# Performance work log

Measured on AMD Instinct MI355X. Metric: run time of the kernel, lower is better.

The kernel has to match this reference:

```python
import jax, jax.numpy as jnp
import numpy as np
from jax import lax

KERNEL_SIZE = 15  # conv padding = kernel_size, kernel width = 2*kernel_size+1


def setup_inputs() -> dict:
    key = jax.random.key(0)
    ks = jax.random.split(key, 11)
    B, T, H, U, KN = 32, 2048, 1024, 1024, 32
    inp = {
        "query": jax.random.normal(ks[0], (1, B, H), dtype=jnp.float32),
        "values": jax.random.normal(ks[1], (B, T, H), dtype=jnp.float32),
        "prev_att": jax.random.uniform(ks[2], (B, 1, T), dtype=jnp.float32),
        "W1_w": jax.random.normal(ks[3], (U, H), dtype=jnp.float32) * 0.02,
        "W1_b": jax.random.normal(ks[4], (U,), dtype=jnp.float32) * 0.02,
        "W2_w": jax.random.normal(ks[5], (U, H), dtype=jnp.float32) * 0.02,
        "W2_b": jax.random.normal(ks[6], (U,), dtype=jnp.float32) * 0.02,
        "V_w": jax.random.normal(ks[7], (1, U), dtype=jnp.float32) * 0.02,
        "V_b": jax.random.normal(ks[8], (1,), dtype=jnp.float32) * 0.02,
        "conv_w": jax.random.normal(ks[9], (KN, 1, 2 * KERNEL_SIZE + 1), dtype=jnp.float32) * 0.02,
        "loc_proj_w": jax.random.normal(ks[10], (U, KN), dtype=jnp.float32) * 0.02,
    }
    return inp


def reference(query, values, prev_att, W1_w, W1_b, W2_w, W2_b, V_w, V_b, conv_w, loc_proj_w):
    # query: [1,B,H] -> [B,H]
    q = jnp.squeeze(query, axis=0)
    hidden_with_time_axis = q[:, None, :]  # [B,1,H]

    # location features: Conv1d over prev attention [B,1,T] -> [B,KN,T]
    loc = lax.conv_general_dilated(
        prev_att, conv_w,
        window_strides=(1,),
        padding=[(KERNEL_SIZE, KERNEL_SIZE)],
        dimension_numbers=("NCH", "OIH", "NCH"),
    )
    # project KN -> units: [B,T,U]
    loc_context = jnp.einsum("bkt,uk->btu", loc, loc_proj_w)

    # W1(values) [B,T,U] + W2(query) [B,1,U] + loc_context [B,T,U]
    sum_1 = (jnp.einsum("bth,uh->btu", values, W1_w) + W1_b
             + jnp.einsum("bh,uh->bu", q, W2_w)[:, None, :] + W2_b
             + loc_context)

    # score: [B,T,1]
    score = jnp.einsum("btu,ou->bto", jnp.tanh(sum_1), V_w) + V_b
    attention_weights = jax.nn.softmax(score, axis=1)  # softmax over time
    context_vector = jnp.sum(attention_weights * values, axis=1)  # [B,H]
    return (context_vector, attention_weights, score)
```

## Files before the change

### kernel.cpp

```cpp
#include <hip/hip_runtime.h>
#include <cstdint>
#include <cstddef>

typedef unsigned short ushort_t;
typedef __attribute__((ext_vector_type(8))) short short8;
typedef __attribute__((ext_vector_type(4))) float floatx4;

#define B_   32
#define T_   2048
#define H_   1024
#define U_   1024
#define KN_  32
#define KEXT 1056
#define BT_  (B_ * T_)

__device__ __forceinline__ unsigned short f2bf(float f) {
    union { float f; unsigned int u; } v; v.f = f;
    unsigned int u = v.u;
    return (unsigned short)((u + 0x7FFFu + ((u >> 16) & 1u)) >> 16);
}
__device__ __forceinline__ float bf2f(unsigned short h) {
    union { unsigned int u; float f; } v; v.u = ((unsigned int)h) << 16;
    return v.f;
}
__device__ __forceinline__ float bflo(unsigned int u) {
    union { unsigned int u; float f; } v; v.u = u << 16; return v.f;
}
__device__ __forceinline__ float bfhi(unsigned int u) {
    union { unsigned int u; float f; } v; v.u = u & 0xffff0000u; return v.f;
}
__device__ __forceinline__ void async_cp16(const void* g, void* l) {
    __builtin_amdgcn_global_load_lds(
        (const __attribute__((address_space(1))) unsigned int*)g,
        (__attribute__((address_space(3))) unsigned int*)l, 16, 0, 0);
}
__device__ __forceinline__ float fast_tanh(float x) {
    float e = __expf(2.0f * x);
    return 1.0f - 2.0f * __builtin_amdgcn_rcpf(e + 1.0f);
}

__global__ void pack_values(const float* __restrict__ values, ushort_t* __restrict__ A) {
    const int tid = threadIdx.x;
    const size_t base = (size_t)blockIdx.x * 8;
#pragma unroll
    for (int r = 0; r < 8; ++r) {
        const size_t row = base + r;
        float4 v = reinterpret_cast<const float4*>(values + row * H_)[tid];
        ushort4 o;
        o.x = f2bf(v.x); o.y = f2bf(v.y); o.z = f2bf(v.z); o.w = f2bf(v.w);
        *reinterpret_cast<ushort4*>(A + row * KEXT + tid * 4) = o;
    }
}

__global__ void conv_pack(const float* __restrict__ prev, const float* __restrict__ convw,
                          ushort_t* __restrict__ A) {
    __shared__ float satt[158];
    __shared__ float sw[KN_ * 31];
    const int tid = threadIdx.x;
    const int b = blockIdx.y, t0 = blockIdx.x * 128;
    for (int i = tid; i < 158; i += 256) {
        int t = t0 - 15 + i;
        satt[i] = (t >= 0 && t < T_) ? prev[b * T_ + t] : 0.0f;
    }
    for (int i = tid; i < KN_ * 31; i += 256) sw[i] = convw[i];
    __syncthreads();
    for (int idx = tid; idx < 128 * KN_; idx += 256) {
        const int k = idx & 31, tl = idx >> 5;
        float acc = 0.0f;
#pragma unroll
        for (int j = 0; j < 31; ++j) acc += satt[tl + j] * sw[k * 31 + j];
        A[(size_t)(b * T_ + t0 + tl) * KEXT + H_ + k] = f2bf(acc);
    }
}

__global__ void pack_w_bias(const float* __restrict__ W1w, const float* __restrict__ locp,
                            const float* __restrict__ W2w, const float* __restrict__ q,
                            const float* __restrict__ W1b, const float* __restrict__ W2b,
                            ushort_t* __restrict__ Bm, float* __restrict__ bias) {
    const int u = blockIdx.x, tid = threadIdx.x;
    float4 v = reinterpret_cast<const float4*>(W1w + (size_t)u * H_)[tid];
    ushort4 o;
    o.x = f2bf(v.x); o.y = f2bf(v.y); o.z = f2bf(v.z); o.w = f2bf(v.w);
    *reinterpret_cast<ushort4*>(Bm + (size_t)u * KEXT + tid * 4) = o;
    if (tid < 8) {
        float4 w = reinterpret_cast<const float4*>(locp + u * KN_)[tid];
        ushort4 o2;
        o2.x = f2bf(w.x); o2.y = f2bf(w.y); o2.z = f2bf(w.z); o2.w = f2bf(w.w);
        *reinterpret_cast<ushort4*>(Bm + (size_t)u * KEXT + H_ + tid * 4) = o2;
    }
    const int lane = tid & 63, wave = tid >> 6;
    const float* wr = W2w + (size_t)u * H_;
    float wv[16];
#pragma unroll
    for (int i = 0; i < 16; ++i) wv[i] = wr[lane + i * 64];
    const float bb = W1b[u] + W2b[u];
#pragma unroll
    for (int j = 0; j < 8; ++j) {
        const int b = wave * 8 + j;
        const float* qr = q + b * H_;
        float acc = 0.0f;
#pragma unroll
        for (int i = 0; i < 16; ++i) acc += wv[i] * qr[lane + i * 64];
#pragma unroll
        for (int off = 32; off >= 1; off >>= 1) acc += __shfl_xor(acc, off, 64);
        if (lane == 0) bias[b * U_ + u] = acc + bb;
    }
}

__global__ __launch_bounds__(256, 2)
void score_gemm(const ushort_t* __restrict__ A, const ushort_t* __restrict__ Bm,
                const float* __restrict__ bias, const float* __restrict__ Vw,
                float* __restrict__ sacc) {
    __shared__ __align__(16) ushort_t lA[128 * 32];
    __shared__ __align__(16) ushort_t lB[128 * 32];
    const int tid  = threadIdx.x;
    const int wave = tid >> 6;
    const int lane = tid & 63;

    const int hid  = blockIdx.x;
    const int xcd  = hid & 7;
    const int slot = hid >> 3;
    const int n_idx = slot & 7;
    const int m_idx = ((slot >> 3) << 3) | xcd;
    const int m0 = m_idx * 128;
    const int n0 = n_idx * 128;

    const int wm = (wave >> 1) * 64;
    const int wn = (wave & 1) * 64;
    const int lr   = lane & 15;
    const int quad = lane >> 4;

    floatx4 acc[4][4] = {};

    const ushort_t* Abase = A + (size_t)m0 * KEXT;
    const ushort_t* Bbase = Bm + (size_t)n0 * KEXT;

    const int chunk0 = wave * 64 + lane;
    const int chunk1 = (4 + wave) * 64 + lane;
    const int r0 = chunk0 >> 2, c0 = chunk0 & 3;
    const int r1 = chunk1 >> 2, c1 = chunk1 & 3;

    for (int kk = 0; kk < 33; ++kk) {
        const int kb = kk * 32;
        async_cp16(Abase + (size_t)r0 * KEXT + kb + c0 * 8, lA + wave * 512);
        async_cp16(Abase + (size_t)r1 * KEXT + kb + c1 * 8, lA + (4 + wave) * 512);
        async_cp16(Bbase + (size_t)r0 * KEXT + kb + c0 * 8, lB + wave * 512);
        async_cp16(Bbase + (size_t)r1 * KEXT + kb + c1 * 8, lB + (4 + wave) * 512);
        __syncthreads();

        short8 af[4], bfr[4];
#pragma unroll
        for (int mi = 0; mi < 4; ++mi)
            af[mi] = *reinterpret_cast<const short8*>(lA + (wm + mi * 16 + lr) * 32 + quad * 8);
#pragma unroll
        for (int ni = 0; ni < 4; ++ni)
            bfr[ni] = *reinterpret_cast<const short8*>(lB + (wn + ni * 16 + lr) * 32 + quad * 8);
#pragma unroll
        for (int mi = 0; mi < 4; ++mi)
#pragma unroll
            for (int ni = 0; ni < 4; ++ni)
                acc[mi][ni] = __builtin_amdgcn_mfma_f32_16x16x32_bf16(af[mi], bfr[ni], acc[mi][ni], 0, 0, 0);
        __syncthreads();
    }

    const int b = m0 >> 11;
    const float* brow = bias + b * U_;
    float vw[4], bv[4];
#pragma unroll
    for (int ni = 0; ni < 4; ++ni) {
        const int u = n0 + wn + ni * 16 + lr;
        vw[ni] = Vw[u];
        bv[ni] = brow[u];
    }
#pragma unroll
    for (int mi = 0; mi < 4; ++mi) {
#pragma unroll
        for (int r = 0; r < 4; ++r) {
            float s = 0.0f;
#pragma unroll
            for (int ni = 0; ni < 4; ++ni)
                s += vw[ni] * fast_tanh(acc[mi][ni][r] + bv[ni]);
            s += __shfl_xor(s, 1, 64);
            s += __shfl_xor(s, 2, 64);
            s += __shfl_xor(s, 4, 64);
            s += __shfl_xor(s, 8, 64);
            if (lr == 0)
                atomicAdd(&sacc[m0 + wm + mi * 16 + quad * 4 + r], s);
        }
    }
}

__global__ void softmax_k(const float* __restrict__ sacc, const float* __restrict__ Vb,
                          float* __restrict__ out) {
    const int b = blockIdx.x, tid = threadIdx.x;
    const int lane = tid & 63, wave = tid >> 6;
    const float vb = Vb[0];
    float v[8], e[8];
    float mx = -1e30f;
#pragma unroll
    for (int j = 0; j < 8; ++j) {
        v[j] = sacc[b * T_ + j * 256 + tid] + vb;
        out[98304 + b * T_ + j * 256 + tid] = v[j];
        mx = fmaxf(mx, v[j]);
    }
#pragma unroll
    for (int off = 32; off >= 1; off >>= 1) mx = fmaxf(mx, __shfl_xor(mx, off, 64));
    __shared__ float sm[4], ss[4];
    if (lane == 0) sm[wave] = mx;
    __syncthreads();
    mx = fmaxf(fmaxf(sm[0], sm[1]), fmaxf(sm[2], sm[3]));
    float sum = 0.0f;
#pragma unroll
    for (int j = 0; j < 8; ++j) { e[j] = __expf(v[j] - mx); sum += e[j]; }
#pragma unroll
    for (int off = 32; off >= 1; off >>= 1) sum += __shfl_xor(sum, off, 64);
    if (lane == 0) ss[wave] = sum;
    __syncthreads();
    sum = ss[0] + ss[1] + ss[2] + ss[3];
    const float inv = 1.0f / sum;
#pragma unroll
    for (int j = 0; j < 8; ++j)
        out[32768 + b * T_ + j * 256 + tid] = e[j] * inv;
}

__global__ void context_k(const ushort_t* __restrict__ A, const float* __restrict__ attn,
                          float* __restrict__ ctx) {
    const int b = blockIdx.y, tc = blockIdx.x, tid = threadIdx.x;
    __shared__ float sa[128];
    if (tid < 128) sa[tid] = attn[b * T_ + tc * 128 + tid];
    __syncthreads();
    const int hh = (tid & 127) * 8;
    const int tp = tid >> 7;
    const ushort_t* base = A + (size_t)(b * T_ + tc * 128 + tp) * KEXT + hh;
    float a[8] = {0, 0, 0, 0, 0, 0, 0, 0};
    for (int t = 0; t < 128; t += 2) {
        const float w = sa[t + tp];
        uint4 u = *reinterpret_cast<const uint4*>(base + (size_t)t * KEXT);
        a[0] += w * bflo(u.x); a[1] += w * bfhi(u.x);
        a[2] += w * bflo(u.y); a[3] += w * bfhi(u.y);
        a[4] += w * bflo(u.z); a[5] += w * bfhi(u.z);
        a[6] += w * bflo(u.w); a[7] += w * bfhi(u.w);
    }
#pragma unroll
    for (int j = 0; j < 8; ++j)
        atomicAdd(&ctx[b * H_ + hh + j], a[j]);
}

extern "C" void kernel_launch(void* const* d_in, const int* in_sizes, int n_in,
                              void* d_out, int out_size, void* d_ws, size_t ws_size,
                              hipStream_t stream) {
    const float* query    = (const float*)d_in[0];
    const float* values   = (const float*)d_in[1];
    const float* prev_att = (const float*)d_in[2];
    const float* W1w      = (const float*)d_in[3];
    const float* W1b      = (const float*)d_in[4];
    const float* W2w      = (const float*)d_in[5];
    const float* W2b      = (const float*)d_in[6];
    const float* Vw       = (const float*)d_in[7];
    const float* Vb       = (const float*)d_in[8];
    const float* convw    = (const float*)d_in[9];
    const float* locp     = (const float*)d_in[10];
    float* out = (float*)d_out;

    char* ws = (char*)d_ws;
    ushort_t* A    = (ushort_t*)(ws);
    ushort_t* Bm   = (ushort_t*)(ws + 138412032);
    float*    bias = (float*)(ws + 140574720);
    float*    sacc = (float*)(ws + 140705792);

    hipMemsetAsync(sacc, 0, BT_ * sizeof(float), stream);
    hipMemsetAsync(out, 0, 32768 * sizeof(float), stream);

    pack_values<<<BT_ / 8, 256, 0, stream>>>(values, A);
    conv_pack<<<dim3(16, 32), 256, 0, stream>>>(prev_att, convw, A);
    pack_w_bias<<<1024, 256, 0, stream>>>(W1w, locp, W2w, query, W1b, W2b, Bm, bias);
    score_gemm<<<4096, 256, 0, stream>>>(A, Bm, bias, Vw, sacc);
    softmax_k<<<32, 256, 0, stream>>>(sacc, Vb, out);
    context_k<<<dim3(16, 32), 256, 0, stream>>>(A, out + 32768, out);
}
```

Before: 643.4 us.

## Double K-step per sync in score GEMM and XOR-swizzle LDS layout

```diff
diff --git a/kernel.cpp b/kernel.cpp
--- a/kernel.cpp
+++ b/kernel.cpp
@@ -14,14 +14,10 @@
 #define KEXT 1056
 #define BT_  (B_ * T_)
 
-__device__ __forceinline__ unsigned short f2bf(float f) {
+__device__ __forceinline__ unsigned int f2bf_u(float f) {
     union { float f; unsigned int u; } v; v.f = f;
     unsigned int u = v.u;
-    return (unsigned short)((u + 0x7FFFu + ((u >> 16) & 1u)) >> 16);
-}
-__device__ __forceinline__ float bf2f(unsigned short h) {
-    union { unsigned int u; float f; } v; v.u = ((unsigned int)h) << 16;
-    return v.f;
+    return (u + 0x7FFFu + ((u >> 16) & 1u)) >> 16;
 }
 __device__ __forceinline__ float bflo(unsigned int u) {
     union { unsigned int u; float f; } v; v.u = u << 16; return v.f;
@@ -47,7 +43,8 @@
         const size_t row = base + r;
         float4 v = reinterpret_cast<const float4*>(values + row * H_)[tid];
         ushort4 o;
-        o.x = f2bf(v.x); o.y = f2bf(v.y); o.z = f2bf(v.z); o.w = f2bf(v.w);
+        o.x = (ushort_t)f2bf_u(v.x); o.y = (ushort_t)f2bf_u(v.y);
+        o.z = (ushort_t)f2bf_u(v.z); o.w = (ushort_t)f2bf_u(v.w);
         *reinterpret_cast<ushort4*>(A + row * KEXT + tid * 4) = o;
     }
 }
@@ -69,7 +66,7 @@
         float acc = 0.0f;
 #pragma unroll
         for (int j = 0; j < 31; ++j) acc += satt[tl + j] * sw[k * 31 + j];
-        A[(size_t)(b * T_ + t0 + tl) * KEXT + H_ + k] = f2bf(acc);
+        A[(size_t)(b * T_ + t0 + tl) * KEXT + H_ + k] = (ushort_t)f2bf_u(acc);
     }
 }
 
@@ -78,14 +75,18 @@
                             const float* __restrict__ W1b, const float* __restrict__ W2b,
                             ushort_t* __restrict__ Bm, float* __restrict__ bias) {
     const int u = blockIdx.x, tid = threadIdx.x;
-    float4 v = reinterpret_cast<const float4*>(W1w + (size_t)u * H_)[tid];
-    ushort4 o;
-    o.x = f2bf(v.x); o.y = f2bf(v.y); o.z = f2bf(v.z); o.w = f2bf(v.w);
-    *reinterpret_cast<ushort4*>(Bm + (size_t)u * KEXT + tid * 4) = o;
+    {
+        float4 v = reinterpret_cast<const float4*>(W1w + (size_t)u * H_)[tid];
+        ushort4 o;
+        o.x = (ushort_t)f2bf_u(v.x); o.y = (ushort_t)f2bf_u(v.y);
+        o.z = (ushort_t)f2bf_u(v.z); o.w = (ushort_t)f2bf_u(v.w);
+        *reinterpret_cast<ushort4*>(Bm + (size_t)u * KEXT + tid * 4) = o;
+    }
     if (tid < 8) {
         float4 w = reinterpret_cast<const float4*>(locp + u * KN_)[tid];
         ushort4 o2;
-        o2.x = f2bf(w.x); o2.y = f2bf(w.y); o2.z = f2bf(w.z); o2.w = f2bf(w.w);
+        o2.x = (ushort_t)f2bf_u(w.x); o2.y = (ushort_t)f2bf_u(w.y);
+        o2.z = (ushort_t)f2bf_u(w.z); o2.w = (ushort_t)f2bf_u(w.w);
         *reinterpret_cast<ushort4*>(Bm + (size_t)u * KEXT + H_ + tid * 4) = o2;
     }
     const int lane = tid & 63, wave = tid >> 6;
@@ -111,8 +112,8 @@
 void score_gemm(const ushort_t* __restrict__ A, const ushort_t* __restrict__ Bm,
                 const float* __restrict__ bias, const float* __restrict__ Vw,
                 float* __restrict__ sacc) {
-    __shared__ __align__(16) ushort_t lA[128 * 32];
-    __shared__ __align__(16) ushort_t lB[128 * 32];
+    __shared__ __align__(16) ushort_t lA[128 * 64];
+    __shared__ __align__(16) ushort_t lB[128 * 64];
     const int tid  = threadIdx.x;
     const int wave = tid >> 6;
     const int lane = tid & 63;
@@ -135,32 +136,71 @@
     const ushort_t* Abase = A + (size_t)m0 * KEXT;
     const ushort_t* Bbase = Bm + (size_t)n0 * KEXT;
 
-    const int chunk0 = wave * 64 + lane;
-    const int chunk1 = (4 + wave) * 64 + lane;
-    const int r0 = chunk0 >> 2, c0 = chunk0 & 3;
-    const int r1 = chunk1 >> 2, c1 = chunk1 & 3;
-
-    for (int kk = 0; kk < 33; ++kk) {
-        const int kb = kk * 32;
-        async_cp16(Abase + (size_t)r0 * KEXT + kb + c0 * 8, lA + wave * 512);
-        async_cp16(Abase + (size_t)r1 * KEXT + kb + c1 * 8, lA + (4 + wave) * 512);
-        async_cp16(Bbase + (size_t)r0 * KEXT + kb + c0 * 8, lB + wave * 512);
-        async_cp16(Bbase + (size_t)r1 * KEXT + kb + c1 * 8, lB + (4 + wave) * 512);
+    int srcOff[4];
+#pragma unroll
+    for (int j = 0; j < 4; ++j) {
+        const int s = j * 256 + wave * 64 + lane;
+        const int sub = s >> 9, w = s & 511;
+        const int row = w >> 2;
+        const int c = (w & 3) ^ ((w >> 3) & 3);
+        srcOff[j] = row * KEXT + (sub * 4 + c) * 8;
+    }
+    int srcOffT[2];
+#pragma unroll
+    for (int j = 0; j < 2; ++j) {
+        const int s = j * 256 + wave * 64 + lane;
+        const int row = s >> 2;
+        const int c = (s & 3) ^ ((s >> 3) & 3);
+        srcOffT[j] = row * KEXT + c * 8;
+    }
+    const int cxor = (quad ^ ((lr >> 1) & 3)) * 8;
+
+    for (int kk = 0; kk < 16; ++kk) {
+        const int kb = kk * 64;
+#pragma unroll
+        for (int j = 0; j < 4; ++j) {
+            async_cp16(Abase + kb + srcOff[j], lA + j * 2048 + wave * 512);
+            async_cp16(Bbase + kb + srcOff[j], lB + j * 2048 + wave * 512);
+        }
         __syncthreads();
-
+#pragma unroll
+        for (int half = 0; half < 2; ++half) {
+            const ushort_t* pA = lA + half * 4096;
+            const ushort_t* pB = lB + half * 4096;
+            short8 af[4], bfr[4];
+#pragma unroll
+            for (int mi = 0; mi < 4; ++mi)
+                af[mi] = *reinterpret_cast<const short8*>(pA + (wm + mi * 16 + lr) * 32 + cxor);
+#pragma unroll
+            for (int ni = 0; ni < 4; ++ni)
+                bfr[ni] = *reinterpret_cast<const short8*>(pB + (wn + ni * 16 + lr) * 32 + cxor);
+#pragma unroll
+            for (int mi = 0; mi < 4; ++mi)
+#pragma unroll
+                for (int ni = 0; ni < 4; ++ni)
+                    acc[mi][ni] = __builtin_amdgcn_mfma_f32_16x16x32_bf16(af[mi], bfr[ni], acc[mi][ni], 0, 0, 0);
+        }
+        __syncthreads();
+    }
+    {
+#pragma unroll
+        for (int j = 0; j < 2; ++j) {
+            async_cp16(Abase + 1024 + srcOffT[j], lA + j * 2048 + wave * 512);
+            async_cp16(Bbase + 1024 + srcOffT[j], lB + j * 2048 + wave * 512);
+        }
+        __syncthreads();
         short8 af[4], bfr[4];
 #pragma unroll
         for (int mi = 0; mi < 4; ++mi)
-            af[mi] = *reinterpret_cast<const short8*>(lA + (wm + mi * 16 + lr) * 32 + quad * 8);
+            af[mi] = *reinterpret_cast<const short8*>(lA + (wm + mi * 16 + lr) * 32 + cxor);
 #pragma unroll
         for (int ni = 0; ni < 4; ++ni)
-            bfr[ni] = *reinterpret_cast<const short8*>(lB + (wn + ni * 16 + lr) * 32 + quad * 8);
+            bfr[ni] = *reinterpret_cast<const short8*>(lB + (wn + ni * 16 + lr) * 32 + cxor);
 #pragma unroll
         for (int mi = 0; mi < 4; ++mi)
 #pragma unroll
             for (int ni = 0; ni < 4; ++ni)
                 acc[mi][ni] = __builtin_amdgcn_mfma_f32_16x16x32_bf16(af[mi], bfr[ni], acc[mi][ni], 0, 0, 0);
-        __syncthreads();
     }
 
     const int b = m0 >> 11;
```

Result: no change. 640.4 us (-0.5%).
